# Optimization experiments

Hardware: AMD Instinct MI355X
Metric: run time of the kernel (lower is better)

Reference implementation:

```python
import jax, jax.numpy as jnp
import numpy as np

L = 8          # context_length
P = 196        # patches_per_frame
PT = 16        # patches_per_tactile_frame
N_EMBD = 768
N_HEAD = 12
BATCH = 4
T = (L + 1) + L * PT + L * P  # 1705


def build_mask(L, P, Pt):
    # image-query block rows (L*P rows)
    mi = np.zeros((L * P, L * P))
    a1 = np.zeros((L * P, L + 1))
    t1 = np.zeros((L * P, L * Pt))
    for i in range(L):
        mi[i * P:(i + 1) * P, :(i + 1) * P] = 1
        a1[i * P:(i + 2) * P, :i + 2] = 1
        t1[i * P:(i + 1) * P, :(i + 1) * Pt] = 1
    m1 = np.concatenate([a1, t1, mi], axis=1)
    # tactile-query block rows (L*Pt rows)
    a2 = np.zeros((L * Pt, L + 1))
    t2 = np.zeros((L * Pt, L * Pt))
    i2 = np.zeros((L * Pt, L * P))
    for i in range(L):
        a2[i * Pt:(i + 2) * Pt, :i + 2] = 1
        t2[i * Pt:(i + 1) * Pt, :(i + 1) * Pt] = 1
        i2[i * Pt:(i + 1) * Pt, :(i + 1) * P] = 1
    m2 = np.concatenate([a2, t2, i2], axis=1)
    # action-query rows (L+1 rows)
    a3 = np.zeros((L + 1, L + 1))
    t3 = np.zeros((L + 1, L * Pt))
    i3 = np.zeros((L + 1, L * P))
    for i in range(L + 1):
        a3[i:i + 2, :i + 2] = 1
        t3[i:i + 1, :(i + 1) * Pt] = 1
        i3[i:i + 1, :(i + 1) * P] = 1
    m3 = np.concatenate([a3, t3, i3], axis=1)
    return np.concatenate([m3, m2, m1], axis=0).astype(bool)


def setup_inputs() -> dict:
    key = jax.random.key(0)
    k1, k2, k3 = jax.random.split(key, 3)
    x = jax.random.normal(k1, (BATCH, T, N_EMBD), dtype=jnp.float32)
    W_attn = jax.random.normal(k2, (N_EMBD, 3 * N_EMBD), dtype=jnp.float32) * 0.02
    W_proj = jax.random.normal(k3, (N_EMBD, N_EMBD), dtype=jnp.float32) * 0.02
    mask = jnp.asarray(build_mask(L, P, PT))
    return {"x": x, "W_attn": W_attn, "W_proj": W_proj, "mask": mask, "n_head": N_HEAD}


def reference(x, W_attn, W_proj, mask, n_head):
    B, Tq, C = x.shape
    hd = C // n_head
    qkv = x @ W_attn                      # [B, T, 3C]
    q, k, v = jnp.split(qkv, 3, axis=-1)
    # [B, H, T, hd]
    q = q.reshape(B, Tq, n_head, hd).transpose(0, 2, 1, 3)
    k = k.reshape(B, Tq, n_head, hd).transpose(0, 2, 1, 3)
    v = v.reshape(B, Tq, n_head, hd).transpose(0, 2, 1, 3)
    scores = jnp.einsum("bhqd,bhkd->bhqk", q, k) / jnp.sqrt(jnp.float32(hd))
    scores = jnp.where(mask[None, None, :, :], scores, jnp.float32(-1e9))
    probs = jax.nn.softmax(scores, axis=-1)
    y = jnp.einsum("bhqk,bhkd->bhqd", probs, v)
    y = y.transpose(0, 2, 1, 3).reshape(B, Tq, C)
    return y @ W_proj
```

## Files before the change

### kernel.cpp

```cpp
#include <hip/hip_runtime.h>
#include <hip/hip_bf16.h>

typedef __attribute__((ext_vector_type(8))) short short8;
typedef __attribute__((ext_vector_type(4))) float f32x4;

#define MFMA16(a,b,c) __builtin_amdgcn_mfma_f32_16x16x32_bf16((a),(b),(c),0,0,0)

#define WAITVM(N) asm volatile("s_waitcnt vmcnt(" #N ")" ::: "memory")
#define BAR()     asm volatile("s_barrier" ::: "memory")

constexpr int Tt = 1705;
constexpr int Tp = 1792;
constexpr int NKT_ALL = 28;
constexpr int NH = 12, HD = 64, Bb = 4, C_ = 768;
constexpr int M_  = Bb * Tt;
constexpr int Mp  = 6912;
constexpr int NQT = 14;
constexpr int NCHA = 2;
constexpr float QSCALE = 0.18033688011116016f;

static_assert(Mp % 256 == 0 && (3 * C_) % 256 == 0, "256-tile grid");

__device__ __forceinline__ void gl16(const void* g, void* l) {
  __builtin_amdgcn_global_load_lds((const __attribute__((address_space(1))) void*)g,
                                   (__attribute__((address_space(3))) void*)l, 16, 0, 0);
}

__device__ __forceinline__ float ex2(float x) {
  float r; asm("v_exp_f32 %0, %1" : "=v"(r) : "v"(x)); return r;
}

__device__ __forceinline__ int frame_of(int t) {
  return t < 9 ? t : (t < 137 ? ((t - 9) >> 4) : ((t - 137) / 196));
}

__device__ __forceinline__ int lim16(int a) {
  if (a >= Tt) return 0;
  int bnd = min(a + 15, Tt - 1);
  int fmax = (a == 0) ? 8 : frame_of(min(bnd, a < 137 ? 136 : bnd));
  return (fmax >= 8) ? Tt : 137 + (fmax + 1) * 196;
}

__global__ __launch_bounds__(256) void k_conv_x(const float* __restrict__ x,
                                                __hip_bfloat16* __restrict__ xb) {
  int i = blockIdx.x * 256 + threadIdx.x;
  if (i >= Mp * C_ / 4) return;
  float4 v = make_float4(0.f, 0.f, 0.f, 0.f);
  if (i * 4 < M_ * C_) v = ((const float4*)x)[i];
  __hip_bfloat16 o0 = __float2bfloat16(v.x), o1 = __float2bfloat16(v.y),
                 o2 = __float2bfloat16(v.z), o3 = __float2bfloat16(v.w);
  ushort4 u = make_ushort4(*(unsigned short*)&o0, *(unsigned short*)&o1,
                           *(unsigned short*)&o2, *(unsigned short*)&o3);
  ((ushort4*)xb)[i] = u;
}

__global__ __launch_bounds__(256) void k_transpose_w(const float* __restrict__ src,
                                                     __hip_bfloat16* __restrict__ dst,
                                                     int K, int N) {
  __shared__ float tile[32][33];
  int kb = blockIdx.x * 32, nb = blockIdx.y * 32;
  int tx = threadIdx.x & 31, ty = threadIdx.x >> 5;
  for (int i = 0; i < 4; i++)
    tile[ty + i * 8][tx] = src[(size_t)(kb + ty + i * 8) * N + nb + tx];
  __syncthreads();
  for (int i = 0; i < 4; i++)
    dst[(size_t)(nb + ty + i * 8) * K + kb + tx] = __float2bfloat16(tile[tx][ty + i * 8]);
}

__global__ __launch_bounds__(512) void k_gemm_qkv(const __hip_bfloat16* __restrict__ xb,
                                                  const __hip_bfloat16* __restrict__ wat,
                                                  __hip_bfloat16* __restrict__ q,
                                                  __hip_bfloat16* __restrict__ kpk,
                                                  __hip_bfloat16* __restrict__ vpk) {
  __shared__ __hip_bfloat16 As[4][256 * 32], Bs[4][256 * 32];
  const int tid = threadIdx.x;
  const int lane = tid & 63, w = tid >> 6;
  const int wr = w >> 2, wc = w & 3;
  const int l16 = lane & 15, grp = lane >> 4;
  const int m0 = blockIdx.x * 256, n0 = blockIdx.y * 256;
  constexpr int NT = C_ / 32;

  auto stage = [&](int t, int bb) {
    int k0 = t * 32;
    for (int p = 0; p < 2; p++) {
      int idx = p * 512 + tid;
      int row = idx >> 2;
      int c8 = (idx & 3) ^ ((row >> 1) & 3);
      gl16(xb  + (size_t)(m0 + row) * C_ + k0 + c8 * 8, &As[bb][idx * 8]);
      gl16(wat + (size_t)(n0 + row) * C_ + k0 + c8 * 8, &Bs[bb][idx * 8]);
    }
  };

  f32x4 acc[8][4];
  for (int i = 0; i < 8; i++)
    for (int j = 0; j < 4; j++) { f32x4 z = {0.f,0.f,0.f,0.f}; acc[i][j] = z; }

  stage(0, 0); stage(1, 1); stage(2, 2);

  for (int t = 0; t < NT; t++) {
    if (t + 3 < NT) stage(t + 3, (t + 3) & 3);
    int rem = NT - 1 - t;
    if (rem >= 3)      WAITVM(12);
    else if (rem == 2) WAITVM(8);
    else if (rem == 1) WAITVM(4);
    else               WAITVM(0);
    BAR();
    const __hip_bfloat16* Ac = As[t & 3];
    const __hip_bfloat16* Bc = Bs[t & 3];
    short8 bfr[4], afr[4];
    for (int nj = 0; nj < 4; nj++) {
      int row = wc * 64 + nj * 16 + l16;
      bfr[nj] = *(const short8*)(Bc + row * 32 + ((grp ^ ((row >> 1) & 3)) * 8));
    }
    for (int mi = 0; mi < 4; mi++) {
      int row = wr * 128 + mi * 16 + l16;
      afr[mi] = *(const short8*)(Ac + row * 32 + ((grp ^ ((row >> 1) & 3)) * 8));
    }
    __builtin_amdgcn_s_setprio(1);
    for (int mi = 0; mi < 4; mi++)
      for (int nj = 0; nj < 4; nj++)
        acc[mi][nj] = MFMA16(afr[mi], bfr[nj], acc[mi][nj]);
    __builtin_amdgcn_s_setprio(0);
    for (int mi = 0; mi < 4; mi++) {
      int row = wr * 128 + 64 + mi * 16 + l16;
      afr[mi] = *(const short8*)(Ac + row * 32 + ((grp ^ ((row >> 1) & 3)) * 8));
    }
    __builtin_amdgcn_s_setprio(1);
    for (int mi = 0; mi < 4; mi++)
      for (int nj = 0; nj < 4; nj++)
        acc[4 + mi][nj] = MFMA16(afr[mi], bfr[nj], acc[4 + mi][nj]);
    __builtin_amdgcn_s_setprio(0);
    BAR();
  }

  const int which = n0 / C_;
  const int c0 = n0 - which * C_ + wc * 64;
  for (int mi = 0; mi < 8; mi++)
    for (int r = 0; r < 4; r++) {
      int m = m0 + wr * 128 + mi * 16 + grp * 4 + r;
      if (m >= M_) continue;
      int b = m / Tt, t = m - b * Tt;
      for (int nj = 0; nj < 4; nj++) {
        int c = c0 + nj * 16 + l16;
        int h = c >> 6, d = c & 63;
        float val = acc[mi][nj][r];
        int bh = b * NH + h;
        if (which == 0) {
          q[((size_t)bh * Tp + t) * HD + d] = __float2bfloat16(val * QSCALE);
        } else if (which == 1) {
          int kt = t >> 6, jj = (t >> 4) & 3, mm = t & 15;
          int half = d >> 5, gg = (d >> 3) & 3, ss = d & 7;
          kpk[(((size_t)bh * NKT_ALL + kt) * 8 + jj * 2 + half) * 512 +
              (gg * 16 + mm) * 8 + ss] = __float2bfloat16(val);
        } else {
          int kt = t >> 6, kb2 = (t >> 5) & 1, k32 = t & 31;
          int gg = (k32 >> 2) & 3, ss = (k32 & 3) + ((k32 >> 4) & 1) * 4;
          int jt = d >> 4, mm = d & 15;
          vpk[(((size_t)bh * NKT_ALL + kt) * 8 + jt * 2 + kb2) * 512 +
              (gg * 16 + mm) * 8 + ss] = __float2bfloat16(val);
        }
      }
    }
}

__global__ __launch_bounds__(256) void k_gemm_proj64(const __hip_bfloat16* __restrict__ A,
                                                     const __hip_bfloat16* __restrict__ Bt,
                                                     float* __restrict__ out) {
  __shared__ __hip_bfloat16 As[4][64 * 32], Bs[4][128 * 32];
  const int tid = threadIdx.x;
  const int lane = tid & 63, w = tid >> 6;
  const int l16 = lane & 15, grp = lane >> 4;
  const int m0 = blockIdx.x * 64, n0 = blockIdx.y * 128;
  f32x4 acc[8];
  for (int j = 0; j < 8; j++) { f32x4 z = {0.f,0.f,0.f,0.f}; acc[j] = z; }

  auto stage = [&](int t, int bb) {
    int k0 = t * 32;
    int row = tid >> 2;
    int c8 = (tid & 3) ^ ((row >> 1) & 3);
    gl16(A + (size_t)(m0 + row) * C_ + k0 + c8 * 8, &As[bb][tid * 8]);
    for (int rr = 0; rr < 2; rr++) {
      int idx = rr * 256 + tid;
      int brow = idx >> 2;
      int bc8 = (idx & 3) ^ ((brow >> 1) & 3);
      gl16(Bt + (size_t)(n0 + brow) * C_ + k0 + bc8 * 8, &Bs[bb][idx * 8]);
    }
  };

  constexpr int NT = C_ / 32;
  stage(0, 0); stage(1, 1); stage(2, 2);

  for (int t = 0; t < NT; t++) {
    if (t + 3 < NT) stage(t + 3, (t + 3) & 3);
    int rem = NT - 1 - t;
    if (rem >= 3)      WAITVM(9);
    else if (rem == 2) WAITVM(6);
    else if (rem == 1) WAITVM(3);
    else               WAITVM(0);
    BAR();
    const __hip_bfloat16* Ac = As[t & 3];
    const __hip_bfloat16* Bc = Bs[t & 3];
    int arow = w * 16 + l16;
    short8 a = *(const short8*)(Ac + arow * 32 + ((grp ^ ((arow >> 1) & 3)) * 8));
    __builtin_amdgcn_s_setprio(1);
    for (int j = 0; j < 8; j++) {
      int brow = j * 16 + l16;
      short8 b = *(const short8*)(Bc + brow * 32 + ((grp ^ ((brow >> 1) & 3)) * 8));
      acc[j] = MFMA16(a, b, acc[j]);
    }
    __builtin_amdgcn_s_setprio(0);
    BAR();
  }

  for (int r = 0; r < 4; r++) {
    int m = m0 + w * 16 + grp * 4 + r;
    if (m >= M_) continue;
    for (int j = 0; j < 8; j++)
      out[(size_t)m * C_ + n0 + j * 16 + l16] = acc[j][r];
  }
}

union S8u { short8 v; struct { unsigned long long lo, hi; } q; unsigned u[4]; };

__device__ __forceinline__ unsigned pack2bf(float a, float b) {
  union { __hip_bfloat162 h; unsigned u; } cv;
  cv.h = __float22bfloat162_rn(make_float2(a, b));
  return cv.u;
}

__global__ __launch_bounds__(256, 2) void k_attn(const __hip_bfloat16* __restrict__ q,
                                                 const __hip_bfloat16* __restrict__ kpk,
                                                 const __hip_bfloat16* __restrict__ vpk,
                                                 __hip_bfloat16* __restrict__ Opart,
                                                 float* __restrict__ lpart) {
  const int tid = threadIdx.x, lane = tid & 63, w = tid >> 6;
  const int l16 = lane & 15, grp = lane >> 4;
  const int rp = w >> 1, ch = w & 1;
  const int id = blockIdx.x;
  const int xslot = id & 7, rr_ = id >> 3;
  const int oct = rr_ / NQT;
  const int bh = xslot + 8 * oct;
  const int qt = rr_ - oct * NQT;
  const int t0q = qt * 128;
  const int a0 = t0q + rp * 64;
  const __hip_bfloat16* qb = q + (size_t)bh * Tp * HD;

  int lim[4], Cmn[4], Ath[4], Bth[4], Cth[4];
  for (int g = 0; g < 4; g++) {
    int a = a0 + g * 16;
    lim[g] = lim16(a);
    int fqmn, fql;
    if (a >= Tt) { fqmn = 8; fql = 8; }
    else {
      int bnd = min(a + 15, Tt - 1);
      fqmn = min(frame_of(a), frame_of(bnd));
      int t = a + l16;
      fql = (t >= Tt) ? 8 : frame_of(t);
    }
    Cmn[g] = min(137 + 196 * (fqmn + 1), Tt);
    Ath[g] = fql + 2;
    Bth[g] = 9 + 16 * (fql + 1);
    Cth[g] = min(137 + 196 * (fql + 1), Tt);
  }
  int limw = max(max(lim[0], lim[1]), max(lim[2], lim[3]));
  int nktw = (limw + 63) >> 6;
  int k0t = (ch * nktw) >> 1;
  int k1t = ((ch + 1) * nktw) >> 1;

  short8 qa[4][2];
  for (int g = 0; g < 4; g++) {
    const __hip_bfloat16* qr = qb + (size_t)(a0 + g * 16 + l16) * HD + grp * 8;
    qa[g][0] = *(const short8*)(qr);
    qa[g][1] = *(const short8*)(qr + 32);
  }
  f32x4 o[4][4];
  for (int g = 0; g < 4; g++)
    for (int jt = 0; jt < 4; jt++) { f32x4 z = {0.f,0.f,0.f,0.f}; o[g][jt] = z; }
  f32x4 ps[4];
  for (int g = 0; g < 4; g++) { f32x4 z = {0.f,0.f,0.f,0.f}; ps[g] = z; }

  const short8* kbase = (const short8*)(kpk + (size_t)bh * NKT_ALL * 4096);
  const short8* vbase = (const short8*)(vpk + (size_t)bh * NKT_ALL * 4096);

  for (int kt = k0t; kt < k1t; kt++) {
    const int t0k = kt * 64;
    const short8* kp = kbase + (size_t)kt * 512;
    const short8* vp = vbase + (size_t)kt * 512;
    short8 kf[4][2], vf[4][2];
    for (int j = 0; j < 4; j++)
      for (int hh = 0; hh < 2; hh++) kf[j][hh] = kp[(j * 2 + hh) * 64 + lane];
    for (int jt = 0; jt < 4; jt++)
      for (int kb2 = 0; kb2 < 2; kb2++) vf[jt][kb2] = vp[(jt * 2 + kb2) * 64 + lane];

    const bool fullk = (t0k + 64 <= Tt);
    for (int g = 0; g < 4; g++) {
      if (t0k >= lim[g]) continue;
      f32x4 s[4];
      __builtin_amdgcn_s_setprio(1);
      for (int j = 0; j < 4; j++) {
        f32x4 z = {0.f,0.f,0.f,0.f};
        s[j] = MFMA16(kf[j][0], qa[g][0], z);
        s[j] = MFMA16(kf[j][1], qa[g][1], s[j]);
      }
      __builtin_amdgcn_s_setprio(0);
      bool needm = !(fullk && (t0k >= 192 ? (t0k + 64) <= Cmn[g] : Cmn[g] >= Tt));
      if (needm) {
        for (int j = 0; j < 4; j++)
          for (int r = 0; r < 4; r++) {
            int key = t0k + j * 16 + grp * 4 + r;
            int thr = key < 9 ? Ath[g] : (key < 137 ? Bth[g] : Cth[g]);
            if (key >= thr) s[j][r] = -1e30f;
          }
      }
      f32x4 p[4];
      for (int j = 0; j < 4; j++)
        for (int r = 0; r < 4; r++) p[j][r] = ex2(s[j][r]);
      ps[g] += (p[0] + p[1]) + (p[2] + p[3]);
      S8u pf[2];
      pf[0].u[0] = pack2bf(p[0][0], p[0][1]);
      pf[0].u[1] = pack2bf(p[0][2], p[0][3]);
      pf[0].u[2] = pack2bf(p[1][0], p[1][1]);
      pf[0].u[3] = pack2bf(p[1][2], p[1][3]);
      pf[1].u[0] = pack2bf(p[2][0], p[2][1]);
      pf[1].u[1] = pack2bf(p[2][2], p[2][3]);
      pf[1].u[2] = pack2bf(p[3][0], p[3][1]);
      pf[1].u[3] = pack2bf(p[3][2], p[3][3]);
      __builtin_amdgcn_s_setprio(1);
      for (int jt = 0; jt < 4; jt++)
        for (int kb2 = 0; kb2 < 2; kb2++)
          o[g][jt] = MFMA16(vf[jt][kb2], pf[kb2].v, o[g][jt]);
      __builtin_amdgcn_s_setprio(0);
    }
  }

  float lr[4];
  for (int g = 0; g < 4; g++) {
    float sum = (ps[g][0] + ps[g][1]) + (ps[g][2] + ps[g][3]);
    sum += __shfl_xor(sum, 16);
    sum += __shfl_xor(sum, 32);
    lr[g] = sum;
  }

  const int blk = bh * (NQT * NCHA) + qt * NCHA + ch;
  __hip_bfloat16* op = Opart + (size_t)blk * (128 * 64);
  for (int g = 0; g < 4; g++) {
    int row = rp * 64 + g * 16 + l16;
    for (int jt = 0; jt < 4; jt++) {
      unsigned p01 = pack2bf(o[g][jt][0], o[g][jt][1]);
      unsigned p23 = pack2bf(o[g][jt][2], o[g][jt][3]);
      ushort4 u;
      u.x = p01 & 0xffff; u.y = p01 >> 16; u.z = p23 & 0xffff; u.w = p23 >> 16;
      *(ushort4*)(op + row * 64 + jt * 16 + grp * 4) = u;
    }
    if (grp == 0) lpart[(size_t)blk * 128 + row] = lr[g];
  }
}

__global__ __launch_bounds__(256) void k_combine(const __hip_bfloat16* __restrict__ Opart,
                                                 const float* __restrict__ lpart,
                                                 __hip_bfloat16* __restrict__ y) {
  const int tid = threadIdx.x;
  const int qt = blockIdx.x, bh = blockIdx.y;
  const int b = bh / NH, h = bh - b * NH;
  const int t0q = qt * 128;
  const int blk0 = bh * (NQT * NCHA) + qt * NCHA;
  __shared__ float ls[128];
  if (tid < 128) {
    float s = 0.f;
    for (int c = 0; c < NCHA; c++) s += lpart[(size_t)(blk0 + c) * 128 + tid];
    ls[tid] = (s > 0.f) ? 1.0f / s : 0.f;
  }
  __syncthreads();
  for (int it = 0; it < 4; it++) {
    int e8 = it * 256 + tid;
    int e = e8 * 8;
    int row = e >> 6, d = e & 63;
    int t = t0q + row;
    if (t >= Tt) continue;
    float acc[8] = {0,0,0,0,0,0,0,0};
    for (int c = 0; c < NCHA; c++) {
      short8 vv = *(const short8*)(Opart + (size_t)(blk0 + c) * (128 * 64) + e);
      for (int i = 0; i < 8; i++) {
        union { unsigned u; float f; } cv;
        cv.u = ((unsigned)(unsigned short)vv[i]) << 16;
        acc[i] += cv.f;
      }
    }
    float rinv = ls[row];
    short8 outv;
    for (int i = 0; i < 8; i += 2) {
      unsigned p = pack2bf(acc[i] * rinv, acc[i + 1] * rinv);
      outv[i] = (short)(p & 0xffff);
      outv[i + 1] = (short)(p >> 16);
    }
    *(short8*)(y + (size_t)(b * Tt + t) * C_ + h * 64 + d) = outv;
  }
}

extern "C" void kernel_launch(void* const* d_in, const int* in_sizes, int n_in,
                              void* d_out, int out_size, void* d_ws, size_t ws_size,
                              hipStream_t stream) {
  const float* x  = (const float*)d_in[0];
  const float* Wa = (const float*)d_in[1];
  const float* Wp = (const float*)d_in[2];
  float* out = (float*)d_out;

  char* ws = (char*)d_ws;
  size_t off = 0;
  auto alloc = [&](size_t bytes) { size_t r = off; off += (bytes + 255) & ~(size_t)255; return r; };
  __hip_bfloat16* xb  = (__hip_bfloat16*)(ws + alloc((size_t)Mp * C_ * 2));
  __hip_bfloat16* wat = (__hip_bfloat16*)(ws + alloc((size_t)3 * C_ * C_ * 2));
  __hip_bfloat16* wpt = (__hip_bfloat16*)(ws + alloc((size_t)C_ * C_ * 2));
  __hip_bfloat16* qb  = (__hip_bfloat16*)(ws + alloc((size_t)Bb * NH * Tp * HD * 2));
  __hip_bfloat16* kpk = (__hip_bfloat16*)(ws + alloc((size_t)Bb * NH * NKT_ALL * 4096 * 2));
  __hip_bfloat16* vpk = (__hip_bfloat16*)(ws + alloc((size_t)Bb * NH * NKT_ALL * 4096 * 2));
  __hip_bfloat16* yb  = (__hip_bfloat16*)(ws + alloc((size_t)Mp * C_ * 2));
  __hip_bfloat16* Opart = (__hip_bfloat16*)(ws + alloc((size_t)Bb * NH * NQT * NCHA * 128 * 64 * 2));
  float*          lpart = (float*)(ws + alloc((size_t)Bb * NH * NQT * NCHA * 128 * 4));

  k_conv_x<<<(Mp * C_ / 4 + 255) / 256, 256, 0, stream>>>(x, xb);
  k_transpose_w<<<dim3(C_ / 32, 3 * C_ / 32), 256, 0, stream>>>(Wa, wat, C_, 3 * C_);
  k_transpose_w<<<dim3(C_ / 32, C_ / 32), 256, 0, stream>>>(Wp, wpt, C_, C_);
  k_gemm_qkv<<<dim3(Mp / 256, 3 * C_ / 256), 512, 0, stream>>>(xb, wat, qb, kpk, vpk);
  k_attn<<<dim3(Bb * NH * NQT), 256, 0, stream>>>(qb, kpk, vpk, Opart, lpart);
  k_combine<<<dim3(NQT, Bb * NH), 256, 0, stream>>>(Opart, lpart, yb);
  k_gemm_proj64<<<dim3(Mp / 64, C_ / 128), 256, 0, stream>>>(yb, wpt, out);
}
```

Before: 221.9 us.

## Stage K/V tiles in shared LDS with async prefetch and drop split-KV combine

```diff
diff --git a/kernel.cpp b/kernel.cpp
--- a/kernel.cpp
+++ b/kernel.cpp
@@ -16,7 +16,6 @@
 constexpr int M_  = Bb * Tt;
 constexpr int Mp  = 6912;
 constexpr int NQT = 14;
-constexpr int NCHA = 2;
 constexpr float QSCALE = 0.18033688011116016f;
 
 static_assert(Mp % 256 == 0 && (3 * C_) % 256 == 0, "256-tile grid");
@@ -231,22 +230,26 @@
 __global__ __launch_bounds__(256, 2) void k_attn(const __hip_bfloat16* __restrict__ q,
                                                  const __hip_bfloat16* __restrict__ kpk,
                                                  const __hip_bfloat16* __restrict__ vpk,
-                                                 __hip_bfloat16* __restrict__ Opart,
-                                                 float* __restrict__ lpart) {
+                                                 __hip_bfloat16* __restrict__ y) {
+  __shared__ __hip_bfloat16 Ks[4][4096], Vs[4][4096];
   const int tid = threadIdx.x, lane = tid & 63, w = tid >> 6;
   const int l16 = lane & 15, grp = lane >> 4;
-  const int rp = w >> 1, ch = w & 1;
   const int id = blockIdx.x;
   const int xslot = id & 7, rr_ = id >> 3;
   const int oct = rr_ / NQT;
   const int bh = xslot + 8 * oct;
   const int qt = rr_ - oct * NQT;
   const int t0q = qt * 128;
-  const int a0 = t0q + rp * 64;
+  const int a0 = t0q + w * 32;
+  const int b = bh / NH, h = bh - b * NH;
   const __hip_bfloat16* qb = q + (size_t)bh * Tp * HD;
 
-  int lim[4], Cmn[4], Ath[4], Bth[4], Cth[4];
-  for (int g = 0; g < 4; g++) {
+  int maxlim = 0;
+  for (int g8 = 0; g8 < 8; g8++) maxlim = max(maxlim, lim16(t0q + g8 * 16));
+  const int nktb = (maxlim + 63) >> 6;
+
+  int lim[2], Cmn[2], Ath[2], Bth[2], Cth[2];
+  for (int g = 0; g < 2; g++) {
     int a = a0 + g * 16;
     lim[g] = lim16(a);
     int fqmn, fql;
@@ -262,138 +265,119 @@
     Bth[g] = 9 + 16 * (fql + 1);
     Cth[g] = min(137 + 196 * (fql + 1), Tt);
   }
-  int limw = max(max(lim[0], lim[1]), max(lim[2], lim[3]));
-  int nktw = (limw + 63) >> 6;
-  int k0t = (ch * nktw) >> 1;
-  int k1t = ((ch + 1) * nktw) >> 1;
-
-  short8 qa[4][2];
-  for (int g = 0; g < 4; g++) {
+  const int limw = max(lim[0], lim[1]);
+
+  short8 qa[2][2];
+  for (int g = 0; g < 2; g++) {
     const __hip_bfloat16* qr = qb + (size_t)(a0 + g * 16 + l16) * HD + grp * 8;
     qa[g][0] = *(const short8*)(qr);
     qa[g][1] = *(const short8*)(qr + 32);
   }
-  f32x4 o[4][4];
-  for (int g = 0; g < 4; g++)
+  f32x4 o[2][4];
+  for (int g = 0; g < 2; g++)
     for (int jt = 0; jt < 4; jt++) { f32x4 z = {0.f,0.f,0.f,0.f}; o[g][jt] = z; }
-  f32x4 ps[4];
-  for (int g = 0; g < 4; g++) { f32x4 z = {0.f,0.f,0.f,0.f}; ps[g] = z; }
-
-  const short8* kbase = (const short8*)(kpk + (size_t)bh * NKT_ALL * 4096);
-  const short8* vbase = (const short8*)(vpk + (size_t)bh * NKT_ALL * 4096);
-
-  for (int kt = k0t; kt < k1t; kt++) {
+  f32x4 ps[2];
+  { f32x4 z = {0.f,0.f,0.f,0.f}; ps[0] = z; ps[1] = z; }
+
+  const __hip_bfloat16* kb0 = kpk + (size_t)bh * NKT_ALL * 4096;
+  const __hip_bfloat16* vb0 = vpk + (size_t)bh * NKT_ALL * 4096;
+
+  auto stage = [&](int kt, int bb) {
+    const __hip_bfloat16* kp = kb0 + (size_t)kt * 4096;
+    const __hip_bfloat16* vp = vb0 + (size_t)kt * 4096;
+    for (int p = 0; p < 2; p++) {
+      int e = (p * 256 + tid) * 8;
+      gl16(kp + e, &Ks[bb][e]);
+      gl16(vp + e, &Vs[bb][e]);
+    }
+  };
+
+  stage(0, 0); stage(1, 1); stage(2, 2);
+
+  for (int kt = 0; kt < nktb; kt++) {
+    if (kt + 3 < nktb) stage(kt + 3, (kt + 3) & 3);
+    int rem = nktb - 1 - kt;
+    if (rem >= 3)      WAITVM(12);
+    else if (rem == 2) WAITVM(8);
+    else if (rem == 1) WAITVM(4);
+    else               WAITVM(0);
+    BAR();
     const int t0k = kt * 64;
-    const short8* kp = kbase + (size_t)kt * 512;
-    const short8* vp = vbase + (size_t)kt * 512;
-    short8 kf[4][2], vf[4][2];
-    for (int j = 0; j < 4; j++)
-      for (int hh = 0; hh < 2; hh++) kf[j][hh] = kp[(j * 2 + hh) * 64 + lane];
-    for (int jt = 0; jt < 4; jt++)
-      for (int kb2 = 0; kb2 < 2; kb2++) vf[jt][kb2] = vp[(jt * 2 + kb2) * 64 + lane];
-
-    const bool fullk = (t0k + 64 <= Tt);
-    for (int g = 0; g < 4; g++) {
-      if (t0k >= lim[g]) continue;
-      f32x4 s[4];
-      __builtin_amdgcn_s_setprio(1);
-      for (int j = 0; j < 4; j++) {
-        f32x4 z = {0.f,0.f,0.f,0.f};
-        s[j] = MFMA16(kf[j][0], qa[g][0], z);
-        s[j] = MFMA16(kf[j][1], qa[g][1], s[j]);
+    if (t0k < limw) {
+      const short8* kl = (const short8*)Ks[kt & 3];
+      const short8* vl = (const short8*)Vs[kt & 3];
+      short8 kf[4][2], vf[4][2];
+      for (int j = 0; j < 4; j++)
+        for (int hh = 0; hh < 2; hh++) kf[j][hh] = kl[(j * 2 + hh) * 64 + lane];
+      for (int jt = 0; jt < 4; jt++)
+        for (int kb2 = 0; kb2 < 2; kb2++) vf[jt][kb2] = vl[(jt * 2 + kb2) * 64 + lane];
+
+      const bool fullk = (t0k + 64 <= Tt);
+      for (int g = 0; g < 2; g++) {
+        if (t0k >= lim[g]) continue;
+        f32x4 s[4];
+        __builtin_amdgcn_s_setprio(1);
+        for (int j = 0; j < 4; j++) {
+          f32x4 z = {0.f,0.f,0.f,0.f};
+          s[j] = MFMA16(kf[j][0], qa[g][0], z);
+          s[j] = MFMA16(kf[j][1], qa[g][1], s[j]);
+        }
+        __builtin_amdgcn_s_setprio(0);
+        bool needm = !(fullk && (t0k >= 192 ? (t0k + 64) <= Cmn[g] : Cmn[g] >= Tt));
+        if (needm) {
+          if (t0k >= 192) {
+            for (int j = 0; j < 4; j++)
+              for (int r = 0; r < 4; r++) {
+                int key = t0k + j * 16 + grp * 4 + r;
+                if (key >= Cth[g]) s[j][r] = -1e30f;
+              }
+          } else {
+            for (int j = 0; j < 4; j++)
+              for (int r = 0; r < 4; r++) {
+                int key = t0k + j * 16 + grp * 4 + r;
+                int thr = key < 9 ? Ath[g] : (key < 137 ? Bth[g] : Cth[g]);
+                if (key >= thr) s[j][r] = -1e30f;
+              }
+          }
+        }
+        f32x4 p[4];
+        for (int j = 0; j < 4; j++)
+          for (int r = 0; r < 4; r++) p[j][r] = ex2(s[j][r]);
+        ps[g] += (p[0] + p[1]) + (p[2] + p[3]);
+        S8u pf[2];
+        pf[0].u[0] = pack2bf(p[0][0], p[0][1]);
+        pf[0].u[1] = pack2bf(p[0][2], p[0][3]);
+        pf[0].u[2] = pack2bf(p[1][0], p[1][1]);
+        pf[0].u[3] = pack2bf(p[1][2], p[1][3]);
+        pf[1].u[0] = pack2bf(p[2][0], p[2][1]);
+        pf[1].u[1] = pack2bf(p[2][2], p[2][3]);
+        pf[1].u[2] = pack2bf(p[3][0], p[3][1]);
+        pf[1].u[3] = pack2bf(p[3][2], p[3][3]);
+        __builtin_amdgcn_s_setprio(1);
+        for (int jt = 0; jt < 4; jt++)
+          for (int kb2 = 0; kb2 < 2; kb2++)
+            o[g][jt] = MFMA16(vf[jt][kb2], pf[kb2].v, o[g][jt]);
+        __builtin_amdgcn_s_setprio(0);
       }
-      __builtin_amdgcn_s_setprio(0);
-      bool needm = !(fullk && (t0k >= 192 ? (t0k + 64) <= Cmn[g] : Cmn[g] >= Tt));
-      if (needm) {
-        for (int j = 0; j < 4; j++)
-          for (int r = 0; r < 4; r++) {
-            int key = t0k + j * 16 + grp * 4 + r;
-            int thr = key < 9 ? Ath[g] : (key < 137 ? Bth[g] : Cth[g]);
-            if (key >= thr) s[j][r] = -1e30f;
-          }
-      }
-      f32x4 p[4];
-      for (int j = 0; j < 4; j++)
-        for (int r = 0; r < 4; r++) p[j][r] = ex2(s[j][r]);
-      ps[g] += (p[0] + p[1]) + (p[2] + p[3]);
-      S8u pf[2];
-      pf[0].u[0] = pack2bf(p[0][0], p[0][1]);
-      pf[0].u[1] = pack2bf(p[0][2], p[0][3]);
-      pf[0].u[2] = pack2bf(p[1][0], p[1][1]);
-      pf[0].u[3] = pack2bf(p[1][2], p[1][3]);
-      pf[1].u[0] = pack2bf(p[2][0], p[2][1]);
-      pf[1].u[1] = pack2bf(p[2][2], p[2][3]);
-      pf[1].u[2] = pack2bf(p[3][0], p[3][1]);
-      pf[1].u[3] = pack2bf(p[3][2], p[3][3]);
-      __builtin_amdgcn_s_setprio(1);
-      for (int jt = 0; jt < 4; jt++)
-        for (int kb2 = 0; kb2 < 2; kb2++)
-          o[g][jt] = MFMA16(vf[jt][kb2], pf[kb2].v, o[g][jt]);
-      __builtin_amdgcn_s_setprio(0);
-    }
-  }
-
-  float lr[4];
-  for (int g = 0; g < 4; g++) {
+    }
+    BAR();
+  }
+
+  for (int g = 0; g < 2; g++) {
     float sum = (ps[g][0] + ps[g][1]) + (ps[g][2] + ps[g][3]);
     sum += __shfl_xor(sum, 16);
     sum += __shfl_xor(sum, 32);
-    lr[g] = sum;
-  }
-
-  const int blk = bh * (NQT * NCHA) + qt * NCHA + ch;
-  __hip_bfloat16* op = Opart + (size_t)blk * (128 * 64);
-  for (int g = 0; g < 4; g++) {
-    int row = rp * 64 + g * 16 + l16;
+    float rinv = (sum > 0.f) ? 1.0f / sum : 0.f;
+    int t = a0 + g * 16 + l16;
+    if (t >= Tt) continue;
+    __hip_bfloat16* yr = y + (size_t)(b * Tt + t) * C_ + h * 64;
     for (int jt = 0; jt < 4; jt++) {
-      unsigned p01 = pack2bf(o[g][jt][0], o[g][jt][1]);
-      unsigned p23 = pack2bf(o[g][jt][2], o[g][jt][3]);
+      unsigned p01 = pack2bf(o[g][jt][0] * rinv, o[g][jt][1] * rinv);
+      unsigned p23 = pack2bf(o[g][jt][2] * rinv, o[g][jt][3] * rinv);
       ushort4 u;
       u.x = p01 & 0xffff; u.y = p01 >> 16; u.z = p23 & 0xffff; u.w = p23 >> 16;
-      *(ushort4*)(op + row * 64 + jt * 16 + grp * 4) = u;
-    }
-    if (grp == 0) lpart[(size_t)blk * 128 + row] = lr[g];
-  }
-}
-
-__global__ __launch_bounds__(256) void k_combine(const __hip_bfloat16* __restrict__ Opart,
-                                                 const float* __restrict__ lpart,
-                                                 __hip_bfloat16* __restrict__ y) {
-  const int tid = threadIdx.x;
-  const int qt = blockIdx.x, bh = blockIdx.y;
-  const int b = bh / NH, h = bh - b * NH;
-  const int t0q = qt * 128;
-  const int blk0 = bh * (NQT * NCHA) + qt * NCHA;
-  __shared__ float ls[128];
-  if (tid < 128) {
-    float s = 0.f;
-    for (int c = 0; c < NCHA; c++) s += lpart[(size_t)(blk0 + c) * 128 + tid];
-    ls[tid] = (s > 0.f) ? 1.0f / s : 0.f;
-  }
-  __syncthreads();
-  for (int it = 0; it < 4; it++) {
-    int e8 = it * 256 + tid;
-    int e = e8 * 8;
-    int row = e >> 6, d = e & 63;
-    int t = t0q + row;
-    if (t >= Tt) continue;
-    float acc[8] = {0,0,0,0,0,0,0,0};
-    for (int c = 0; c < NCHA; c++) {
-      short8 vv = *(const short8*)(Opart + (size_t)(blk0 + c) * (128 * 64) + e);
-      for (int i = 0; i < 8; i++) {
-        union { unsigned u; float f; } cv;
-        cv.u = ((unsigned)(unsigned short)vv[i]) << 16;
-        acc[i] += cv.f;
-      }
-    }
-    float rinv = ls[row];
-    short8 outv;
-    for (int i = 0; i < 8; i += 2) {
-      unsigned p = pack2bf(acc[i] * rinv, acc[i + 1] * rinv);
-      outv[i] = (short)(p & 0xffff);
-      outv[i + 1] = (short)(p >> 16);
-    }
-    *(short8*)(y + (size_t)(b * Tt + t) * C_ + h * 64 + d) = outv;
+      *(ushort4*)(yr + jt * 16 + grp * 4) = u;
+    }
   }
 }
 
@@ -415,14 +399,11 @@
   __hip_bfloat16* kpk = (__hip_bfloat16*)(ws + alloc((size_t)Bb * NH * NKT_ALL * 4096 * 2));
   __hip_bfloat16* vpk = (__hip_bfloat16*)(ws + alloc((size_t)Bb * NH * NKT_ALL * 4096 * 2));
   __hip_bfloat16* yb  = (__hip_bfloat16*)(ws + alloc((size_t)Mp * C_ * 2));
-  __hip_bfloat16* Opart = (__hip_bfloat16*)(ws + alloc((size_t)Bb * NH * NQT * NCHA * 128 * 64 * 2));
-  float*          lpart = (float*)(ws + alloc((size_t)Bb * NH * NQT * NCHA * 128 * 4));
 
   k_conv_x<<<(Mp * C_ / 4 + 255) / 256, 256, 0, stream>>>(x, xb);
   k_transpose_w<<<dim3(C_ / 32, 3 * C_ / 32), 256, 0, stream>>>(Wa, wat, C_, 3 * C_);
   k_transpose_w<<<dim3(C_ / 32, C_ / 32), 256, 0, stream>>>(Wp, wpt, C_, C_);
   k_gemm_qkv<<<dim3(Mp / 256, 3 * C_ / 256), 512, 0, stream>>>(xb, wat, qb, kpk, vpk);
-  k_attn<<<dim3(Bb * NH * NQT), 256, 0, stream>>>(qb, kpk, vpk, Opart, lpart);
-  k_combine<<<dim3(NQT, Bb * NH), 256, 0, stream>>>(Opart, lpart, yb);
+  k_attn<<<dim3(Bb * NH * NQT), 256, 0, stream>>>(qb, kpk, vpk, yb);
   k_gemm_proj64<<<dim3(Mp / 64, C_ / 128), 256, 0, stream>>>(yb, wpt, out);
 }
```

New measurement: 226.5 us. 2.1% more time.
